# Kernel optimization log

Measured on AMD Instinct MI355X. Metric: run time of the kernel, lower is better.

## Reference

```python
import jax, jax.numpy as jnp
import numpy as np

B, N, D, S, ITERS = 64, 2048, 256, 8, 3
SCALE = D ** -0.5
EPS_LN = 1e-5

def _ln(x, g, b):
    m = jnp.mean(x, axis=-1, keepdims=True)
    v = jnp.var(x, axis=-1, keepdims=True)
    return (x - m) / jnp.sqrt(v + EPS_LN) * g + b

def setup_inputs() -> dict:
    key = jax.random.key(0)
    ks = jax.random.split(key, 20)
    s = D ** -0.5
    f32 = jnp.float32
    return dict(
        x=jax.random.normal(ks[0], (B, N, D), f32),
        noise=jax.random.normal(ks[1], (B, S, D), f32),
        slots_mu=jax.random.normal(ks[2], (1, 1, D), f32),
        slots_sigma=jax.random.normal(ks[3], (1, 1, D), f32),
        Wq=jax.random.normal(ks[4], (D, D), f32) * s, bq=jnp.zeros((D,), f32),
        Wk=jax.random.normal(ks[5], (D, D), f32) * s, bk=jnp.zeros((D,), f32),
        Wv=jax.random.normal(ks[6], (D, D), f32) * s, bv=jnp.zeros((D,), f32),
        W_ih=jax.random.normal(ks[7], (3 * D, D), f32) * s, b_ih=jnp.zeros((3 * D,), f32),
        W_hh=jax.random.normal(ks[8], (3 * D, D), f32) * s, b_hh=jnp.zeros((3 * D,), f32),
        W1=jax.random.normal(ks[9], (D, D), f32) * s, b1=jnp.zeros((D,), f32),
        W2=jax.random.normal(ks[10], (D, D), f32) * s, b2=jnp.zeros((D,), f32),
        g_in=jnp.ones((D,), f32), be_in=jnp.zeros((D,), f32),
        g_sl=jnp.ones((D,), f32), be_sl=jnp.zeros((D,), f32),
        g_ff=jnp.ones((D,), f32), be_ff=jnp.zeros((D,), f32),
    )

def reference(x, noise, slots_mu, slots_sigma, Wq, bq, Wk, bk, Wv, bv,
              W_ih, b_ih, W_hh, b_hh, W1, b1, W2, b2,
              g_in, be_in, g_sl, be_sl, g_ff, be_ff):
    # slot init: mu + softplus(sigma) * noise  -> [B,S,D]
    slots = slots_mu + jax.nn.softplus(slots_sigma) * noise
    xn = _ln(x, g_in, be_in)
    k = xn @ Wk.T + bk  # [B,N,D]
    v = xn @ Wv.T + bv
    for _ in range(ITERS):
        prev = slots
        q = _ln(slots, g_sl, be_sl) @ Wq.T + bq  # [B,S,D]
        logits = jnp.einsum('bsd,bnd->bsn', q, k) * SCALE
        attn = jax.nn.softmax(logits, axis=-1) + 1e-8  # softmax over inputs, as in source
        attn = attn / jnp.sum(attn, axis=-1, keepdims=True)
        updates = jnp.einsum('bsn,bnd->bsd', attn, v)
        # GRUCell(input=updates, hidden=prev); torch gate order r,z,n
        gi = updates @ W_ih.T + b_ih
        gh = prev @ W_hh.T + b_hh
        ir, iz, i_n = jnp.split(gi, 3, axis=-1)
        hr, hz, h_n = jnp.split(gh, 3, axis=-1)
        r = jax.nn.sigmoid(ir + hr)
        z = jax.nn.sigmoid(iz + hz)
        n = jnp.tanh(i_n + r * h_n)
        slots = (1.0 - z) * n + z * prev
        # residual MLP
        h = jax.nn.relu(_ln(slots, g_ff, be_ff) @ W1.T + b1)
        slots = slots + (h @ W2.T + b2)
    return slots
```

## Files before the change

### kernel.cpp

```cpp
#include <hip/hip_runtime.h>
#include <cstddef>


#define BB 64
#define NN 2048
#define DD 256
#define NCH 8
#define CHK 256
#define NITER 3
#define XPITCH 264

typedef unsigned short u16;
typedef unsigned int u32;
typedef _Float16 h2 __attribute__((ext_vector_type(2)));
typedef _Float16 h4 __attribute__((ext_vector_type(4)));

#if defined(__has_builtin)
#if __has_builtin(__builtin_amdgcn_fdot2)
#define HAS_FDOT2 1
#endif
#endif

#ifdef HAS_FDOT2
#define FDOT2(a,b,c) __builtin_amdgcn_fdot2((a),(b),(c),false)
#else
#define FDOT2(a,b,c) fmaf((float)(a).y,(float)(b).y, fmaf((float)(a).x,(float)(b).x,(c)))
#endif

__device__ __forceinline__ h2 u2h2(u32 v){ union{u32 u; h2 h;} c; c.u=v; return c.h; }

__global__ __launch_bounds__(256) void kA(const float* __restrict__ noise, const float* __restrict__ mu,
                                          const float* __restrict__ sig, float* __restrict__ S,
                                          const float* __restrict__ Wq, const float* __restrict__ Wk,
                                          const float* __restrict__ bq, const float* __restrict__ Wih,
                                          const float* __restrict__ Wv, const float* __restrict__ bv,
                                          const float* __restrict__ bih,
                                          float* __restrict__ Wqk, float* __restrict__ bqk,
                                          float* __restrict__ Wihv, float* __restrict__ bihv){
  __shared__ float col[256];
  const int t = threadIdx.x;
  const int blk = blockIdx.x;
  if(blk < 256){
    col[t] = Wq[t*256 + blk];
    __syncthreads();
    float acc = 0.f;
    #pragma unroll 4
    for(int j=0;j<256;j++) acc += col[j]*Wk[j*256+t];
    Wqk[blk*256+t] = acc * 0.0625f;
  } else if(blk < 1024){
    int c = blk - 256;
    col[t] = Wih[c*256+t];
    __syncthreads();
    float acc = 0.f;
    #pragma unroll 4
    for(int j=0;j<256;j++) acc += col[j]*Wv[j*256+t];
    Wihv[(size_t)c*256+t] = acc;
  } else if(blk < 1536){
    int i = (blk-1024)*256 + t;
    float sg = sig[t];
    float sp = fmaxf(sg, 0.f) + log1pf(expf(-fabsf(sg)));
    S[i] = mu[t] + sp * noise[i];
  } else if(blk == 1536){
    float acc = 0.f;
    for(int j=0;j<256;j++) acc += bq[j]*Wk[j*256+t];
    bqk[t] = acc * 0.0625f;
  } else {
    for(int c=t;c<768;c+=256){
      float acc = 0.f;
      for(int j=0;j<256;j++) acc += Wih[c*256+j]*bv[j];
      bihv[c] = acc + bih[c];
    }
  }
}

__global__ __launch_bounds__(256) void kB(const float* __restrict__ Wihv, const float* __restrict__ Whh,
                                          const float* __restrict__ W1, const float* __restrict__ W2,
                                          float* __restrict__ WihvT, float* __restrict__ WhhT,
                                          float* __restrict__ W1T, float* __restrict__ W2T,
                                          const float* __restrict__ S0, const float* __restrict__ g_sl,
                                          const float* __restrict__ be_sl, const float* __restrict__ Wqk,
                                          const float* __restrict__ bqk, float* __restrict__ Qq){
  __shared__ float tile[64][65];
  __shared__ float lnA[8][256];
  const int blk = blockIdx.x, t = threadIdx.x;
  if(blk < 128){
    const float* src; float* dst; int R, C, tb;
    if(blk < 48){ src=Wihv; dst=WihvT; R=768; C=256; tb=blk; }
    else if(blk < 96){ src=Whh; dst=WhhT; R=768; C=256; tb=blk-48; }
    else if(blk < 112){ src=W1; dst=W1T; R=256; C=256; tb=blk-96; }
    else { src=W2; dst=W2T; R=256; C=256; tb=blk-112; }
    const int tilesC = C/64;
    const int r0 = (tb/tilesC)*64, c0 = (tb%tilesC)*64;
    const int x = t&63, y = t>>6;
    #pragma unroll
    for(int k=0;k<16;k++) tile[y*16+k][x] = src[(size_t)(r0+y*16+k)*C + c0+x];
    __syncthreads();
    #pragma unroll
    for(int k=0;k<16;k++) dst[(size_t)(c0+y*16+k)*R + r0+x] = tile[x][y*16+k];
    return;
  }
  const int w = t>>6, l = t&63;
  const int r0 = (blk-128)*8;
  #pragma unroll
  for(int rr=0; rr<2; rr++){
    int r = w*2 + rr;
    float4 v = *(const float4*)(S0 + (size_t)(r0+r)*256 + l*4);
    float s1 = v.x+v.y+v.z+v.w;
    float s2 = v.x*v.x+v.y*v.y+v.z*v.z+v.w*v.w;
    #pragma unroll
    for(int off=1; off<64; off<<=1){ s1 += __shfl_xor(s1,off); s2 += __shfl_xor(s2,off); }
    float m = s1*(1.f/256.f);
    float var = s2*(1.f/256.f) - m*m;
    float rs = rsqrtf(var + 1e-5f);
    float4 gg = *(const float4*)(g_sl + l*4);
    float4 bb = *(const float4*)(be_sl + l*4);
    float4 o;
    o.x=(v.x-m)*rs*gg.x+bb.x; o.y=(v.y-m)*rs*gg.y+bb.y;
    o.z=(v.z-m)*rs*gg.z+bb.z; o.w=(v.w-m)*rs*gg.w+bb.w;
    *(float4*)(&lnA[r][l*4]) = o;
  }
  __syncthreads();
  const int c4 = l*4;
  float acc[2][4] = {};
  #pragma unroll 2
  for(int k=0;k<256;k++){
    float4 wv = *(const float4*)(Wqk + (size_t)k*256 + c4);
    float a0 = lnA[2*w][k], a1 = lnA[2*w+1][k];
    acc[0][0]+=a0*wv.x; acc[0][1]+=a0*wv.y; acc[0][2]+=a0*wv.z; acc[0][3]+=a0*wv.w;
    acc[1][0]+=a1*wv.x; acc[1][1]+=a1*wv.y; acc[1][2]+=a1*wv.z; acc[1][3]+=a1*wv.w;
  }
  float4 bq4 = *(const float4*)(bqk + c4);
  #pragma unroll
  for(int rr=0; rr<2; rr++){
    float4 o;
    o.x=acc[rr][0]+bq4.x; o.y=acc[rr][1]+bq4.y; o.z=acc[rr][2]+bq4.z; o.w=acc[rr][3]+bq4.w;
    *(float4*)(Qq + (size_t)(r0+2*w+rr)*256 + c4) = o;
  }
}

__global__ __launch_bounds__(512) void k_attn(const float* __restrict__ x, const float* __restrict__ g_in,
                                              const float* __restrict__ be_in, const float* __restrict__ Qq,
                                              float* __restrict__ mP, float* __restrict__ lP,
                                              float* __restrict__ aP){
  __shared__ __align__(16) u16 xs[256*XPITCH];
  __shared__ h2 qs[8][128];
  __shared__ float plT[8][256];
  __shared__ float mS[8], lS[8];
  const int b = blockIdx.x, c = blockIdx.y, t = threadIdx.x;
  const int w = t>>6, l = t&63;
  {
    const float* xb = x + ((size_t)b*NN + (size_t)c*CHK)*DD;
    float4 gg = *(const float4*)(g_in + l*4);
    float4 bb = *(const float4*)(be_in + l*4);
    #pragma unroll 4
    for(int k=0;k<32;k++){
      int row = w + 8*k;
      float4 v = *(const float4*)(xb + (size_t)row*256 + l*4);
      float s1 = v.x+v.y+v.z+v.w;
      float s2 = v.x*v.x + v.y*v.y + v.z*v.z + v.w*v.w;
      #pragma unroll
      for(int off=1; off<64; off<<=1){ s1 += __shfl_xor(s1,off); s2 += __shfl_xor(s2,off); }
      float m = s1*(1.f/256.f);
      float var = s2*(1.f/256.f) - m*m;
      float rs = rsqrtf(var + 1e-5f);
      union { h4 h; uint2 u2v; } pk;
      pk.h[0] = (_Float16)((v.x-m)*rs*gg.x + bb.x);
      pk.h[1] = (_Float16)((v.y-m)*rs*gg.y + bb.y);
      pk.h[2] = (_Float16)((v.z-m)*rs*gg.z + bb.z);
      pk.h[3] = (_Float16)((v.w-m)*rs*gg.w + bb.w);
      *(uint2*)(xs + (size_t)row*XPITCH + l*4) = pk.u2v;
    }
  }
  for(int i=t; i<1024; i+=512){
    int s = i>>7, p = i&127;
    float a = Qq[b*2048 + s*256 + 2*p];
    float bq = Qq[b*2048 + s*256 + 2*p + 1];
    h2 hv; hv.x = (_Float16)a; hv.y = (_Float16)bq;
    qs[s][p] = hv;
  }
  __syncthreads();
  const int n = t & 255, sg = t >> 8;
  float lg[4]={0,0,0,0};
  {
    const u16* xr = xs + (size_t)n*XPITCH;
    #pragma unroll 4
    for(int d8=0; d8<32; ++d8){
      uint4 u = *(const uint4*)(xr + d8*8);
      h2 xa=u2h2(u.x), xb=u2h2(u.y), xc=u2h2(u.z), xd=u2h2(u.w);
      #pragma unroll
      for(int k=0;k<4;k++){
        const h2* qp = &qs[sg*4+k][d8*4];
        float acc = lg[k];
        acc = FDOT2(xa, qp[0], acc);
        acc = FDOT2(xb, qp[1], acc);
        acc = FDOT2(xc, qp[2], acc);
        acc = FDOT2(xd, qp[3], acc);
        lg[k] = acc;
      }
    }
    #pragma unroll
    for(int k=0;k<4;k++) plT[sg*4+k][n] = lg[k];
  }
  __syncthreads();
  {
    float mx = -1e30f;
    #pragma unroll
    for(int k=0;k<4;k++) mx = fmaxf(mx, plT[w][l + 64*k]);
    #pragma unroll
    for(int off=1; off<64; off<<=1) mx = fmaxf(mx, __shfl_xor(mx, off));
    if(l==0) mS[w] = mx;
  }
  __syncthreads();
  #pragma unroll
  for(int k=0;k<4;k++) plT[sg*4+k][n] = __expf(lg[k] - mS[sg*4+k]);
  __syncthreads();
  {
    float sm = 0.f;
    #pragma unroll
    for(int k=0;k<4;k++) sm += plT[w][l + 64*k];
    #pragma unroll
    for(int off=1; off<64; off<<=1) sm += __shfl_xor(sm, off);
    if(l==0) lS[w] = sm;
  }
  __syncthreads();
  const size_t pb = (size_t)(b*NCH + c)*8;
  {
    float4 a4 = {0.f,0.f,0.f,0.f};
    const u16* xq = xs + 4*l;
    #pragma unroll 8
    for(int nn=0; nn<256; ++nn){
      uint2 u = *(const uint2*)(xq + (size_t)nn*XPITCH);
      h2 ha=u2h2(u.x), hb=u2h2(u.y);
      float p = plT[w][nn];
      a4.x += p*(float)ha.x; a4.y += p*(float)ha.y;
      a4.z += p*(float)hb.x; a4.w += p*(float)hb.y;
    }
    *(float4*)(aP + (pb + w)*256 + l*4) = a4;
  }
  if(t<8){ mP[pb+t] = mS[t]; lP[pb+t] = lS[t]; }
}

union PostU {
  float Gt[2][4][768];
  struct { float Row[4][256]; float Ht[4][256]; float Lq[4][256]; } m;
};

__global__ __launch_bounds__(512) void k_post(const float* __restrict__ mP, const float* __restrict__ lP,
                                              const float* __restrict__ aP, const float* __restrict__ WihvT,
                                              const float* __restrict__ bihv, const float* __restrict__ WhhT,
                                              const float* __restrict__ bhh, const float* __restrict__ Sc,
                                              const float* __restrict__ g_ff, const float* __restrict__ be_ff,
                                              const float* __restrict__ W1T, const float* __restrict__ b1,
                                              const float* __restrict__ W2T, const float* __restrict__ b2,
                                              const float* __restrict__ g_sl, const float* __restrict__ be_sl,
                                              const float* __restrict__ Wqk, const float* __restrict__ bqk,
                                              float* __restrict__ Sout, float* __restrict__ Qq, int writeQ){
  __shared__ float Ut[4][256];
  __shared__ float Sp[4][256];
  __shared__ float Hp[2][4][256];
  __shared__ PostU uu;
  __shared__ float red2[4][2];
  const int t = threadIdx.x;
  const int r0 = blockIdx.x*4;
  const int b = r0>>3;
  const int w = t>>6, l = t&63;
  const int c = t&255, hh = t>>8;

  #pragma unroll
  for(int k=0;k<2;k++){
    int idx = t + 512*k;
    int r = idx>>8, cc = idx&255;
    int rr = r0 + r, ss = rr&7;
    const float* mpb = mP + b*64 + ss;
    const float* lpb = lP + b*64 + ss;
    float M = -1e30f;
    #pragma unroll
    for(int c8=0;c8<8;c8++) M = fmaxf(M, mpb[c8*8]);
    float wc[8]; float L = 0.f;
    #pragma unroll
    for(int c8=0;c8<8;c8++){ wc[c8] = __expf(mpb[c8*8] - M); L += lpb[c8*8]*wc[c8]; }
    float inv = 1.f/L;
    size_t base = ((size_t)b*64 + ss)*256 + cc;
    float u = 0.f;
    #pragma unroll
    for(int c8=0;c8<8;c8++) u += wc[c8]*aP[base + (size_t)c8*2048];
    Ut[r][cc] = u*inv;
    Sp[r][cc] = Sc[(size_t)rr*256 + cc];
  }
  __syncthreads();

  if(t < 384){
    const int mat = t/192, q4 = (t - mat*192)*4;
    const float* WT = mat ? WhhT : WihvT;
    const float* bb2 = mat ? bhh : bihv;
    const float (*A)[256] = mat ? Sp : Ut;
    float4 bias4 = *(const float4*)(bb2 + q4);
    float4 ac0 = bias4, ac1 = bias4, ac2 = bias4, ac3 = bias4;
    const float* wp = WT + q4;
    #pragma unroll 4
    for(int d=0; d<256; ++d){
      float4 wv = *(const float4*)(wp + (size_t)d*768);
      float a0=A[0][d], a1=A[1][d], a2=A[2][d], a3=A[3][d];
      ac0.x += a0*wv.x; ac0.y += a0*wv.y; ac0.z += a0*wv.z; ac0.w += a0*wv.w;
      ac1.x += a1*wv.x; ac1.y += a1*wv.y; ac1.z += a1*wv.z; ac1.w += a1*wv.w;
      ac2.x += a2*wv.x; ac2.y += a2*wv.y; ac2.z += a2*wv.z; ac2.w += a2*wv.w;
      ac3.x += a3*wv.x; ac3.y += a3*wv.y; ac3.z += a3*wv.z; ac3.w += a3*wv.w;
    }
    *(float4*)(&uu.Gt[mat][0][q4]) = ac0;
    *(float4*)(&uu.Gt[mat][1][q4]) = ac1;
    *(float4*)(&uu.Gt[mat][2][q4]) = ac2;
    *(float4*)(&uu.Gt[mat][3][q4]) = ac3;
  }
  __syncthreads();

  #pragma unroll
  for(int k=0;k<2;k++){
    int idx = t + 512*k;
    int r = idx>>8, cc = idx&255;
    float gir = uu.Gt[0][r][cc], giz = uu.Gt[0][r][256+cc], gin = uu.Gt[0][r][512+cc];
    float ghr = uu.Gt[1][r][cc], ghz = uu.Gt[1][r][256+cc], ghn = uu.Gt[1][r][512+cc];
    float rr2 = 1.f/(1.f + __expf(-(gir+ghr)));
    float zz = 1.f/(1.f + __expf(-(giz+ghz)));
    float nn = tanhf(gin + rr2*ghn);
    Ut[r][cc] = (1.f-zz)*nn + zz*Sp[r][cc];
  }
  __syncthreads();

  if(w < 4){
    float s1=0.f, s2=0.f;
    #pragma unroll
    for(int k2=0;k2<4;k2++){ float v = Ut[w][l + 64*k2]; s1 += v; s2 += v*v; }
    #pragma unroll
    for(int off=1; off<64; off<<=1){ s1 += __shfl_xor(s1,off); s2 += __shfl_xor(s2,off); }
    if(l==0){
      float m = s1*(1.f/256.f);
      float var = s2*(1.f/256.f) - m*m;
      red2[w][0] = m; red2[w][1] = rsqrtf(var + 1e-5f);
    }
  }
  __syncthreads();
  #pragma unroll
  for(int k=0;k<2;k++){
    int idx = t + 512*k;
    int r = idx>>8, cc = idx&255;
    uu.m.Row[r][cc] = (Ut[r][cc]-red2[r][0])*red2[r][1]*g_ff[cc] + be_ff[cc];
  }
  __syncthreads();

  {
    const float* w1 = W1T + (size_t)hh*128*256 + c;
    float a0 = hh ? 0.f : b1[c], a1=a0, a2=a0, a3=a0;
    const int dB = hh*128;
    #pragma unroll 8
    for(int d=0; d<128; ++d){
      float wv = w1[(size_t)d*256];
      a0 += uu.m.Row[0][dB+d]*wv;
      a1 += uu.m.Row[1][dB+d]*wv;
      a2 += uu.m.Row[2][dB+d]*wv;
      a3 += uu.m.Row[3][dB+d]*wv;
    }
    Hp[hh][0][c]=a0; Hp[hh][1][c]=a1; Hp[hh][2][c]=a2; Hp[hh][3][c]=a3;
  }
  __syncthreads();
  #pragma unroll
  for(int k=0;k<2;k++){
    int idx = t + 512*k;
    int r = idx>>8, cc = idx&255;
    uu.m.Ht[r][cc] = fmaxf(Hp[0][r][cc]+Hp[1][r][cc], 0.f);
  }
  __syncthreads();

  {
    const float* w2 = W2T + (size_t)hh*128*256 + c;
    float a0 = hh ? 0.f : b2[c], a1=a0, a2=a0, a3=a0;
    const int dB = hh*128;
    #pragma unroll 8
    for(int d=0; d<128; ++d){
      float wv = w2[(size_t)d*256];
      a0 += uu.m.Ht[0][dB+d]*wv;
      a1 += uu.m.Ht[1][dB+d]*wv;
      a2 += uu.m.Ht[2][dB+d]*wv;
      a3 += uu.m.Ht[3][dB+d]*wv;
    }
    Hp[hh][0][c]=a0; Hp[hh][1][c]=a1; Hp[hh][2][c]=a2; Hp[hh][3][c]=a3;
  }
  __syncthreads();
  if(t < 256){
    #pragma unroll
    for(int r=0;r<4;r++){
      float sn = Hp[0][r][c] + Hp[1][r][c] + Ut[r][c];
      Sout[(size_t)(r0+r)*256 + c] = sn;
      Ut[r][c] = sn;
    }
  }

  if(writeQ){
    __syncthreads();
    if(w < 4){
      float s1=0.f, s2=0.f;
      #pragma unroll
      for(int k2=0;k2<4;k2++){ float v = Ut[w][l + 64*k2]; s1 += v; s2 += v*v; }
      #pragma unroll
      for(int off=1; off<64; off<<=1){ s1 += __shfl_xor(s1,off); s2 += __shfl_xor(s2,off); }
      if(l==0){
        float m = s1*(1.f/256.f);
        float var = s2*(1.f/256.f) - m*m;
        red2[w][0] = m; red2[w][1] = rsqrtf(var + 1e-5f);
      }
    }
    __syncthreads();
    #pragma unroll
    for(int k=0;k<2;k++){
      int idx = t + 512*k;
      int r = idx>>8, cc = idx&255;
      uu.m.Lq[r][cc] = (Ut[r][cc]-red2[r][0])*red2[r][1]*g_sl[cc] + be_sl[cc];
    }
    __syncthreads();
    {
      const float* wq = Wqk + (size_t)hh*128*256 + c;
      float a0 = hh ? 0.f : bqk[c], a1=a0, a2=a0, a3=a0;
      const int dB = hh*128;
      #pragma unroll 8
      for(int d=0; d<128; ++d){
        float wv = wq[(size_t)d*256];
        a0 += uu.m.Lq[0][dB+d]*wv;
        a1 += uu.m.Lq[1][dB+d]*wv;
        a2 += uu.m.Lq[2][dB+d]*wv;
        a3 += uu.m.Lq[3][dB+d]*wv;
      }
      Hp[hh][0][c]=a0; Hp[hh][1][c]=a1; Hp[hh][2][c]=a2; Hp[hh][3][c]=a3;
    }
    __syncthreads();
    if(t < 256){
      #pragma unroll
      for(int r=0;r<4;r++)
        Qq[(size_t)(r0+r)*256 + c] = Hp[0][r][c] + Hp[1][r][c];
    }
  }
}

extern "C" void kernel_launch(void* const* d_in, const int* in_sizes, int n_in,
                              void* d_out, int out_size, void* d_ws, size_t ws_size,
                              hipStream_t stream){
  const float* x    = (const float*)d_in[0];
  const float* noise= (const float*)d_in[1];
  const float* mu   = (const float*)d_in[2];
  const float* sig  = (const float*)d_in[3];
  const float* Wq   = (const float*)d_in[4];
  const float* bq   = (const float*)d_in[5];
  const float* Wk   = (const float*)d_in[6];
  const float* Wv   = (const float*)d_in[8];
  const float* bv   = (const float*)d_in[9];
  const float* W_ih = (const float*)d_in[10];
  const float* b_ih = (const float*)d_in[11];
  const float* W_hh = (const float*)d_in[12];
  const float* b_hh = (const float*)d_in[13];
  const float* W1m  = (const float*)d_in[14];
  const float* b1v  = (const float*)d_in[15];
  const float* W2m  = (const float*)d_in[16];
  const float* b2v  = (const float*)d_in[17];
  const float* g_in = (const float*)d_in[18];
  const float* be_in= (const float*)d_in[19];
  const float* g_sl = (const float*)d_in[20];
  const float* be_sl= (const float*)d_in[21];
  const float* g_ff = (const float*)d_in[22];
  const float* be_ff= (const float*)d_in[23];

  char* p = (char*)d_ws;
  auto alloc = [&](size_t bytes)->char*{ char* q = p; p += (bytes + 255) & ~(size_t)255; return q; };
  float* Wqk   = (float*)alloc(256*256*4);
  float* bqk   = (float*)alloc(256*4);
  float* Wihv  = (float*)alloc((size_t)768*256*4);
  float* WihvT = (float*)alloc((size_t)256*768*4);
  float* bihv  = (float*)alloc(768*4);
  float* WhhT  = (float*)alloc((size_t)256*768*4);
  float* W1T   = (float*)alloc(256*256*4);
  float* W2T   = (float*)alloc(256*256*4);
  float* S0    = (float*)alloc(512*256*4);
  float* S1    = (float*)alloc(512*256*4);
  float* Qq    = (float*)alloc(512*256*4);
  float* mP    = (float*)alloc(64*NCH*8*4);
  float* lP    = (float*)alloc(64*NCH*8*4);
  float* aP    = (float*)alloc((size_t)64*NCH*8*256*4);
  if((size_t)(p - (char*)d_ws) > ws_size) return;

  kA<<<1538, 256, 0, stream>>>(noise, mu, sig, S0, Wq, Wk, bq, W_ih, Wv, bv, b_ih,
                               Wqk, bqk, Wihv, bihv);
  kB<<<192, 256, 0, stream>>>(Wihv, W_hh, W1m, W2m, WihvT, WhhT, W1T, W2T,
                              S0, g_sl, be_sl, Wqk, bqk, Qq);

  float* Sin = S0;
  float* Sping[2] = { S1, S0 };
  for(int it=0; it<NITER; ++it){
    float* Sout = (it==NITER-1) ? (float*)d_out : Sping[it&1];
    k_attn<<<dim3(64, NCH), 512, 0, stream>>>(x, g_in, be_in, Qq, mP, lP, aP);
    k_post<<<128, 512, 0, stream>>>(mP, lP, aP, WihvT, bihv, WhhT, b_hh, Sin, g_ff, be_ff,
                                    W1T, b1v, W2T, b2v, g_sl, be_sl, Wqk, bqk,
                                    Sout, Qq, (it<NITER-1) ? 1 : 0);
    Sin = Sout;
  }
}
```

Before: 355.1 us.

## Cache normalized fp16 inputs across iterations and halve attention chunk size

The first attention pass layer-normalizes x and writes it to a workspace buffer as fp16. Later iterations load that buffer directly, so they read half the bytes and skip the LayerNorm recomputation. The chunk size also drops from 256 to 128 rows, doubling the number of blocks and cutting shared memory per block, which should help occupancy. The cost is a 64MB fp16 write in the first iteration and twice as many partial results for the post kernel to merge.

```diff
diff --git a/kernel.cpp b/kernel.cpp
--- a/kernel.cpp
+++ b/kernel.cpp
@@ -5,8 +5,8 @@
 #define BB 64
 #define NN 2048
 #define DD 256
-#define NCH 8
-#define CHK 256
+#define NCH 16
+#define CHK 128
 #define NITER 3
 #define XPITCH 264
 
@@ -138,22 +138,87 @@
   }
 }
 
-__global__ __launch_bounds__(512) void k_attn(const float* __restrict__ x, const float* __restrict__ g_in,
-                                              const float* __restrict__ be_in, const float* __restrict__ Qq,
-                                              float* __restrict__ mP, float* __restrict__ lP,
-                                              float* __restrict__ aP){
-  __shared__ __align__(16) u16 xs[256*XPITCH];
+__device__ __forceinline__ void attn_core(u16* xs, h2 (*qs)[128], float (*plT)[128],
+                                          float* mS, float* lS,
+                                          const float* __restrict__ Qq,
+                                          float* __restrict__ mP, float* __restrict__ lP,
+                                          float* __restrict__ aP, int b, int c, int t){
+  const int w = t>>6, l = t&63;
+  const int n = t & 127, sg = t >> 7;
+  float lg[2]={0,0};
+  {
+    const u16* xr = xs + (size_t)n*XPITCH;
+    #pragma unroll 4
+    for(int d8=0; d8<32; ++d8){
+      uint4 u = *(const uint4*)(xr + d8*8);
+      h2 xa=u2h2(u.x), xb=u2h2(u.y), xc=u2h2(u.z), xd=u2h2(u.w);
+      #pragma unroll
+      for(int k=0;k<2;k++){
+        const h2* qp = &qs[sg*2+k][d8*4];
+        float acc = lg[k];
+        acc = FDOT2(xa, qp[0], acc);
+        acc = FDOT2(xb, qp[1], acc);
+        acc = FDOT2(xc, qp[2], acc);
+        acc = FDOT2(xd, qp[3], acc);
+        lg[k] = acc;
+      }
+    }
+    #pragma unroll
+    for(int k=0;k<2;k++) plT[sg*2+k][n] = lg[k];
+  }
+  __syncthreads();
+  {
+    float mx = fmaxf(plT[w][l], plT[w][l+64]);
+    #pragma unroll
+    for(int off=1; off<64; off<<=1) mx = fmaxf(mx, __shfl_xor(mx, off));
+    if(l==0) mS[w] = mx;
+  }
+  __syncthreads();
+  #pragma unroll
+  for(int k=0;k<2;k++) plT[sg*2+k][n] = __expf(lg[k] - mS[sg*2+k]);
+  __syncthreads();
+  {
+    float sm = plT[w][l] + plT[w][l+64];
+    #pragma unroll
+    for(int off=1; off<64; off<<=1) sm += __shfl_xor(sm, off);
+    if(l==0) lS[w] = sm;
+  }
+  __syncthreads();
+  const size_t pb = (size_t)(b*NCH + c)*8;
+  {
+    float4 a4 = {0.f,0.f,0.f,0.f};
+    const u16* xq = xs + 4*l;
+    #pragma unroll 8
+    for(int nn=0; nn<128; ++nn){
+      uint2 u = *(const uint2*)(xq + (size_t)nn*XPITCH);
+      h2 ha=u2h2(u.x), hb=u2h2(u.y);
+      float p = plT[w][nn];
+      a4.x += p*(float)ha.x; a4.y += p*(float)ha.y;
+      a4.z += p*(float)hb.x; a4.w += p*(float)hb.y;
+    }
+    *(float4*)(aP + (pb + w)*256 + l*4) = a4;
+  }
+  if(t<8){ mP[pb+t] = mS[t]; lP[pb+t] = lS[t]; }
+}
+
+__global__ __launch_bounds__(512) void k_attn0(const float* __restrict__ x, const float* __restrict__ g_in,
+                                               const float* __restrict__ be_in, u16* __restrict__ xn,
+                                               const float* __restrict__ Qq,
+                                               float* __restrict__ mP, float* __restrict__ lP,
+                                               float* __restrict__ aP){
+  __shared__ __align__(16) u16 xs[CHK*XPITCH];
   __shared__ h2 qs[8][128];
-  __shared__ float plT[8][256];
+  __shared__ float plT[8][128];
   __shared__ float mS[8], lS[8];
   const int b = blockIdx.x, c = blockIdx.y, t = threadIdx.x;
   const int w = t>>6, l = t&63;
   {
-    const float* xb = x + ((size_t)b*NN + (size_t)c*CHK)*DD;
+    const size_t rowbase = (size_t)b*NN + (size_t)c*CHK;
+    const float* xb = x + rowbase*DD;
     float4 gg = *(const float4*)(g_in + l*4);
     float4 bb = *(const float4*)(be_in + l*4);
     #pragma unroll 4
-    for(int k=0;k<32;k++){
+    for(int k=0;k<16;k++){
       int row = w + 8*k;
       float4 v = *(const float4*)(xb + (size_t)row*256 + l*4);
       float s1 = v.x+v.y+v.z+v.w;
@@ -169,6 +234,7 @@
       pk.h[2] = (_Float16)((v.z-m)*rs*gg.z + bb.z);
       pk.h[3] = (_Float16)((v.w-m)*rs*gg.w + bb.w);
       *(uint2*)(xs + (size_t)row*XPITCH + l*4) = pk.u2v;
+      *(uint2*)(xn + (rowbase+row)*DD + l*4) = pk.u2v;
     }
   }
   for(int i=t; i<1024; i+=512){
@@ -179,65 +245,35 @@
     qs[s][p] = hv;
   }
   __syncthreads();
-  const int n = t & 255, sg = t >> 8;
-  float lg[4]={0,0,0,0};
-  {
-    const u16* xr = xs + (size_t)n*XPITCH;
-    #pragma unroll 4
-    for(int d8=0; d8<32; ++d8){
-      uint4 u = *(const uint4*)(xr + d8*8);
-      h2 xa=u2h2(u.x), xb=u2h2(u.y), xc=u2h2(u.z), xd=u2h2(u.w);
-      #pragma unroll
-      for(int k=0;k<4;k++){
-        const h2* qp = &qs[sg*4+k][d8*4];
-        float acc = lg[k];
-        acc = FDOT2(xa, qp[0], acc);
-        acc = FDOT2(xb, qp[1], acc);
-        acc = FDOT2(xc, qp[2], acc);
-        acc = FDOT2(xd, qp[3], acc);
-        lg[k] = acc;
-      }
-    }
-    #pragma unroll
-    for(int k=0;k<4;k++) plT[sg*4+k][n] = lg[k];
-  }
-  __syncthreads();
-  {
-    float mx = -1e30f;
-    #pragma unroll
-    for(int k=0;k<4;k++) mx = fmaxf(mx, plT[w][l + 64*k]);
-    #pragma unroll
-    for(int off=1; off<64; off<<=1) mx = fmaxf(mx, __shfl_xor(mx, off));
-    if(l==0) mS[w] = mx;
-  }
-  __syncthreads();
-  #pragma unroll
-  for(int k=0;k<4;k++) plT[sg*4+k][n] = __expf(lg[k] - mS[sg*4+k]);
-  __syncthreads();
-  {
-    float sm = 0.f;
-    #pragma unroll
-    for(int k=0;k<4;k++) sm += plT[w][l + 64*k];
-    #pragma unroll
-    for(int off=1; off<64; off<<=1) sm += __shfl_xor(sm, off);
-    if(l==0) lS[w] = sm;
-  }
-  __syncthreads();
-  const size_t pb = (size_t)(b*NCH + c)*8;
-  {
-    float4 a4 = {0.f,0.f,0.f,0.f};
-    const u16* xq = xs + 4*l;
-    #pragma unroll 8
-    for(int nn=0; nn<256; ++nn){
-      uint2 u = *(const uint2*)(xq + (size_t)nn*XPITCH);
-      h2 ha=u2h2(u.x), hb=u2h2(u.y);
-      float p = plT[w][nn];
-      a4.x += p*(float)ha.x; a4.y += p*(float)ha.y;
-      a4.z += p*(float)hb.x; a4.w += p*(float)hb.y;
-    }
-    *(float4*)(aP + (pb + w)*256 + l*4) = a4;
-  }
-  if(t<8){ mP[pb+t] = mS[t]; lP[pb+t] = lS[t]; }
+  attn_core(xs, qs, plT, mS, lS, Qq, mP, lP, aP, b, c, t);
+}
+
+__global__ __launch_bounds__(512) void k_attnN(const u16* __restrict__ xn, const float* __restrict__ Qq,
+                                               float* __restrict__ mP, float* __restrict__ lP,
+                                               float* __restrict__ aP){
+  __shared__ __align__(16) u16 xs[CHK*XPITCH];
+  __shared__ h2 qs[8][128];
+  __shared__ float plT[8][128];
+  __shared__ float mS[8], lS[8];
+  const int b = blockIdx.x, c = blockIdx.y, t = threadIdx.x;
+  {
+    const uint4* xg4 = (const uint4*)(xn + ((size_t)b*NN + (size_t)c*CHK)*DD);
+    #pragma unroll
+    for(int k=0;k<8;k++){
+      int idx = t + 512*k;
+      int n = idx>>5, j = idx&31;
+      *(uint4*)(xs + (size_t)n*XPITCH + j*8) = xg4[idx];
+    }
+  }
+  for(int i=t; i<1024; i+=512){
+    int s = i>>7, p = i&127;
+    float a = Qq[b*2048 + s*256 + 2*p];
+    float bq = Qq[b*2048 + s*256 + 2*p + 1];
+    h2 hv; hv.x = (_Float16)a; hv.y = (_Float16)bq;
+    qs[s][p] = hv;
+  }
+  __syncthreads();
+  attn_core(xs, qs, plT, mS, lS, Qq, mP, lP, aP, b, c, t);
 }
 
 union PostU {
@@ -271,19 +307,19 @@
     int idx = t + 512*k;
     int r = idx>>8, cc = idx&255;
     int rr = r0 + r, ss = rr&7;
-    const float* mpb = mP + b*64 + ss;
-    const float* lpb = lP + b*64 + ss;
+    const float* mpb = mP + b*(NCH*8) + ss;
+    const float* lpb = lP + b*(NCH*8) + ss;
     float M = -1e30f;
     #pragma unroll
-    for(int c8=0;c8<8;c8++) M = fmaxf(M, mpb[c8*8]);
-    float wc[8]; float L = 0.f;
-    #pragma unroll
-    for(int c8=0;c8<8;c8++){ wc[c8] = __expf(mpb[c8*8] - M); L += lpb[c8*8]*wc[c8]; }
+    for(int c8=0;c8<NCH;c8++) M = fmaxf(M, mpb[c8*8]);
+    float wc[NCH]; float L = 0.f;
+    #pragma unroll
+    for(int c8=0;c8<NCH;c8++){ wc[c8] = __expf(mpb[c8*8] - M); L += lpb[c8*8]*wc[c8]; }
     float inv = 1.f/L;
-    size_t base = ((size_t)b*64 + ss)*256 + cc;
+    size_t base = ((size_t)b*(NCH*8) + ss)*256 + cc;
     float u = 0.f;
     #pragma unroll
-    for(int c8=0;c8<8;c8++) u += wc[c8]*aP[base + (size_t)c8*2048];
+    for(int c8=0;c8<NCH;c8++) u += wc[c8]*aP[base + (size_t)c8*2048];
     Ut[r][cc] = u*inv;
     Sp[r][cc] = Sc[(size_t)rr*256 + cc];
   }
@@ -468,6 +504,7 @@
 
   char* p = (char*)d_ws;
   auto alloc = [&](size_t bytes)->char*{ char* q = p; p += (bytes + 255) & ~(size_t)255; return q; };
+  u16*   xn    = (u16*)  alloc((size_t)BB*NN*DD*2);
   float* Wqk   = (float*)alloc(256*256*4);
   float* bqk   = (float*)alloc(256*4);
   float* Wihv  = (float*)alloc((size_t)768*256*4);
@@ -493,7 +530,10 @@
   float* Sping[2] = { S1, S0 };
   for(int it=0; it<NITER; ++it){
     float* Sout = (it==NITER-1) ? (float*)d_out : Sping[it&1];
-    k_attn<<<dim3(64, NCH), 512, 0, stream>>>(x, g_in, be_in, Qq, mP, lP, aP);
+    if(it == 0)
+      k_attn0<<<dim3(64, NCH), 512, 0, stream>>>(x, g_in, be_in, xn, Qq, mP, lP, aP);
+    else
+      k_attnN<<<dim3(64, NCH), 512, 0, stream>>>(xn, Qq, mP, lP, aP);
     k_post<<<128, 512, 0, stream>>>(mP, lP, aP, WihvT, bihv, WhhT, b_hh, Sin, g_ff, be_ff,
                                     W1T, b1v, W2T, b2v, g_sl, be_sl, Wqk, bqk,
                                     Sout, Qq, (it<NITER-1) ? 1 : 0);
```

Result: faster. 313.7 us (-11.6%).
